# Kernel optimization log

Measured on AMD Instinct MI355X. Metric: run time of the kernel, lower is better.

The kernel has to match this reference:

```python
import jax, jax.numpy as jnp
import numpy as np

SEQ, B, I, H, O = 512, 256, 256, 512, 256


def setup_inputs() -> dict:
    key = jax.random.key(0)
    ks = jax.random.split(key, 7)
    s_ih = 1.0 / np.sqrt(H)
    return {
        "x_seq": jax.random.normal(ks[0], (SEQ, B, I), dtype=jnp.float32),
        # PyTorch LSTMCell params: gate order i, f, g, o
        "W_ih": jax.random.uniform(ks[1], (4 * H, I), jnp.float32, -s_ih, s_ih),
        "W_hh": jax.random.uniform(ks[2], (4 * H, H), jnp.float32, -s_ih, s_ih),
        "b_ih": jax.random.uniform(ks[3], (4 * H,), jnp.float32, -s_ih, s_ih),
        "b_hh": jax.random.uniform(ks[4], (4 * H,), jnp.float32, -s_ih, s_ih),
        "W_fc": jax.random.uniform(ks[5], (O, H), jnp.float32, -s_ih, s_ih),
        "b_fc": jax.random.uniform(ks[6], (O,), jnp.float32, -s_ih, s_ih),
    }


def reference(x_seq, W_ih, W_hh, b_ih, b_hh, W_fc, b_fc):
    hidden = W_hh.shape[1]
    # Precompute input projections for all timesteps at once: [S, B, 4H]
    x_proj = jnp.einsum("sbi,gi->sbg", x_seq, W_ih) + b_ih + b_hh

    def step(carry, xp_t):
        h, c = carry
        gates = xp_t + h @ W_hh.T  # [B, 4H]
        i_g, f_g, g_g, o_g = jnp.split(gates, 4, axis=-1)
        i_g = jax.nn.sigmoid(i_g)
        f_g = jax.nn.sigmoid(f_g)
        g_g = jnp.tanh(g_g)
        o_g = jax.nn.sigmoid(o_g)
        c = f_g * c + i_g * g_g
        h = o_g * jnp.tanh(c)
        return (h, c), h

    h0 = jnp.zeros((x_seq.shape[1], hidden), x_seq.dtype)
    c0 = jnp.zeros_like(h0)
    (h_f, c_f), hs = jax.lax.scan(step, (h0, c0), x_proj)
    # Linear head applied to every timestep's hidden state: [S, B, O]
    outputs = jnp.einsum("sbh,oh->sbo", hs, W_fc) + b_fc
    return outputs, (h_f, c_f)
```

## Files before the change

kernel.cpp:

```cpp
#include <hip/hip_runtime.h>
#include <math.h>

#define SEQ   512
#define BATCH 256
#define IDIM  256
#define HDIM  512
#define ODIM  256
#define NGROUP 16
#define GBLK   16

#define OUT_ELEMS ((size_t)SEQ * BATCH * ODIM)
#define HF_OFF OUT_ELEMS
#define CF_OFF (OUT_ELEMS + (size_t)BATCH * HDIM)

#define HPLANE     65536u
#define HBUFSTRIDE 131072u
#define SPIN_TIMEOUT 200000000ull

#define H_SCALE 4096.0f
#define H_INV   2.44140625e-4f
#define HMIN    6.104e-5f
#define ZW      390

typedef __attribute__((ext_vector_type(8))) _Float16 half8;
typedef __attribute__((ext_vector_type(4))) float f32x4;
typedef __attribute__((ext_vector_type(4))) unsigned int uint4v;

__device__ __forceinline__ unsigned short hbits(_Float16 h) {
  return __builtin_bit_cast(unsigned short, h);
}

__device__ __forceinline__ f32x4 mfma_h(half8 a, half8 b, f32x4 c) {
  return __builtin_amdgcn_mfma_f32_16x16x32_f16(a, b, c, 0, 0, 0);
}

__device__ __forceinline__ unsigned int ld_sys_u32(const unsigned int* p) {
  unsigned int v;
  asm volatile("global_load_dword %0, %1, off sc0 sc1\n\t"
               "s_waitcnt vmcnt(0)"
               : "=v"(v) : "v"((unsigned long long)p) : "memory");
  return v;
}

__device__ __forceinline__ void st_sys_u32(unsigned int* p, unsigned int d) {
  asm volatile("global_store_dword %0, %1, off sc0 sc1"
               : : "v"((unsigned long long)p), "v"(d) : "memory");
}

__device__ __forceinline__ void ld_2x64_sys(const unsigned int* p0, const unsigned int* p1,
                                            uint4v a[4], uint4v b[4]) {
  asm volatile(
      "global_load_dwordx4 %0, %8, off sc0 sc1\n\t"
      "global_load_dwordx4 %1, %8, off offset:16 sc0 sc1\n\t"
      "global_load_dwordx4 %2, %8, off offset:32 sc0 sc1\n\t"
      "global_load_dwordx4 %3, %8, off offset:48 sc0 sc1\n\t"
      "global_load_dwordx4 %4, %9, off sc0 sc1\n\t"
      "global_load_dwordx4 %5, %9, off offset:16 sc0 sc1\n\t"
      "global_load_dwordx4 %6, %9, off offset:32 sc0 sc1\n\t"
      "global_load_dwordx4 %7, %9, off offset:48 sc0 sc1\n\t"
      "s_waitcnt vmcnt(0)"
      : "=&v"(a[0]), "=&v"(a[1]), "=&v"(a[2]), "=&v"(a[3]),
        "=&v"(b[0]), "=&v"(b[1]), "=&v"(b[2]), "=&v"(b[3])
      : "v"((unsigned long long)p0), "v"((unsigned long long)p1)
      : "memory");
}

__device__ __forceinline__ void split_f(float f, _Float16 &hi, _Float16 &lo) {
  _Float16 a = (_Float16)0.f;
  if (fabsf(f) >= HMIN) a = (_Float16)f;
  float f1 = (float)a;
  hi = a;
  lo = (_Float16)((f - f1) * H_SCALE);
}

__device__ __forceinline__ float sigm(float x)   { return 1.f / (1.f + expf(-x)); }
__device__ __forceinline__ float tanh_f(float x) { return 1.f - 2.f / (expf(2.f * x) + 1.f); }

__device__ __forceinline__ void wait_tag(const unsigned int* tp, unsigned int tgt) {
  unsigned long long t0 = __builtin_amdgcn_s_memrealtime();
  while (ld_sys_u32(tp) < tgt) {
    if (__builtin_amdgcn_s_memrealtime() - t0 > SPIN_TIMEOUT) break;
  }
}

__global__ void __launch_bounds__(256, 1)
lstm_mfma(const float* __restrict__ xs,
          const float* __restrict__ Wih,
          const float* __restrict__ Whh,
          const float* __restrict__ bih,
          const float* __restrict__ bhh,
          const float* __restrict__ Wfc,
          const float* __restrict__ bfc,
          float* __restrict__ out,
          unsigned int* __restrict__ tags,
          unsigned int* __restrict__ hb)
{
  const int tid = threadIdx.x;
  const int w   = tid >> 6;
  const int l   = tid & 63;
  const int lr  = l & 15;
  const int lk  = l >> 4;

  const int bi  = blockIdx.x & (NGROUP - 1);
  const int gj  = blockIdx.x / NGROUP;
  const int r0  = bi * 16;
  const int hc0 = gj * 32;
  const int oc0 = gj * 16;

  half8 wz1[24][2], wz2[24][2];
#pragma unroll
  for (int kk = 0; kk < 24; ++kk)
#pragma unroll
    for (int nt = 0; nt < 2; ++nt) {
      int g = w * HDIM + hc0 + nt * 16 + lr;
      const float* src = (kk < 16)
          ? (Whh + (size_t)g * HDIM + kk * 32 + lk * 8)
          : (Wih + (size_t)g * IDIM + (kk - 16) * 32 + lk * 8);
      const f32x4 va = *(const f32x4*)src;
      const f32x4 vb = *(const f32x4*)(src + 4);
#pragma unroll
      for (int j = 0; j < 4; ++j) { _Float16 h, lo; split_f(va[j], h, lo); wz1[kk][nt][j] = h; wz2[kk][nt][j] = lo; }
#pragma unroll
      for (int j = 0; j < 4; ++j) { _Float16 h, lo; split_f(vb[j], h, lo); wz1[kk][nt][4 + j] = h; wz2[kk][nt][4 + j] = lo; }
    }
  half8 wfc1[4];
#pragma unroll
  for (int q = 0; q < 4; ++q) {
    const float* src = Wfc + (size_t)(oc0 + lr) * HDIM + (w * 4 + q) * 32 + lk * 8;
#pragma unroll
    for (int j = 0; j < 8; ++j) { _Float16 h, lo; split_f(src[j], h, lo); wfc1[q][j] = h; }
  }
  float gb[2];
#pragma unroll
  for (int nt = 0; nt < 2; ++nt) {
    int g = w * HDIM + hc0 + nt * 16 + lr;
    gb[nt] = bih[g] + bhh[g];
  }

  const int rrow = tid >> 4;
  const int rcp  = tid & 15;
  const float fcb = bfc[oc0 + rcp];

  __shared__ unsigned int z1[16][ZW];
  __shared__ unsigned int z2[16][ZW];
  __shared__ float lds_g[4][16][32];
  __shared__ float lds_fc[4][16][16];
  __shared__ float lds_c[16][32];

  lds_c[rrow][2 * rcp]     = 0.f;
  lds_c[rrow][2 * rcp + 1] = 0.f;

  const int srow = tid & 15;
  const int schk = tid >> 4;
  unsigned int* mytag = tags + (bi * 16 + schk) * 4;

#pragma unroll 1
  for (int t = 0; t < SEQ; ++t) {
    {
      const float* xt = xs + (size_t)t * BATCH * IDIM + (size_t)(r0 + srow) * IDIM + schk * 16;
#pragma unroll
      for (int i = 0; i < 8; ++i) {
        _Float16 h0, l0, h1, l1;
        split_f(xt[2 * i],     h0, l0);
        split_f(xt[2 * i + 1], h1, l1);
        int c = 256 + schk * 8 + i;
        z1[srow][c] = (unsigned int)hbits(h0) | ((unsigned int)hbits(h1) << 16);
        z2[srow][c] = (unsigned int)hbits(l0) | ((unsigned int)hbits(l1) << 16);
      }
    }

    if (t > 0) {
      wait_tag(mytag, (unsigned int)t);
      const unsigned int* p1 = hb + ((unsigned)((t - 1) & 1)) * HBUFSTRIDE
                             + (unsigned)(r0 + srow) * 256u + (unsigned)(schk * 16);
      uint4v a[4], b[4];
      ld_2x64_sys(p1, p1 + HPLANE, a, b);
#pragma unroll
      for (int j = 0; j < 4; ++j)
#pragma unroll
        for (int e = 0; e < 4; ++e) {
          z1[srow][schk * 16 + 4 * j + e] = a[j][e];
          z2[srow][schk * 16 + 4 * j + e] = b[j][e];
        }
    } else {
#pragma unroll
      for (int i = 0; i < 16; ++i) {
        z1[srow][schk * 16 + i] = 0u;
        z2[srow][schk * 16 + i] = 0u;
      }
    }
    __syncthreads();

    f32x4 ga0 = {gb[0], gb[0], gb[0], gb[0]};
    f32x4 ga1 = {gb[1], gb[1], gb[1], gb[1]};
    f32x4 gl0 = {0.f, 0.f, 0.f, 0.f};
    f32x4 gl1 = {0.f, 0.f, 0.f, 0.f};
    const unsigned short* zr1 = (const unsigned short*)&z1[lr][0];
    const unsigned short* zr2 = (const unsigned short*)&z2[lr][0];
#pragma unroll
    for (int kk = 0; kk < 24; ++kk) {
      half8 a1 = *(const half8*)(zr1 + kk * 32 + lk * 8);
      half8 a2 = *(const half8*)(zr2 + kk * 32 + lk * 8);
      ga0 = mfma_h(a1, wz1[kk][0], ga0);
      gl0 = mfma_h(a2, wz1[kk][0], gl0);
      gl0 = mfma_h(a1, wz2[kk][0], gl0);
      ga1 = mfma_h(a1, wz1[kk][1], ga1);
      gl1 = mfma_h(a2, wz1[kk][1], gl1);
      gl1 = mfma_h(a1, wz2[kk][1], gl1);
    }

    f32x4 f1a = {0.f, 0.f, 0.f, 0.f};
    f32x4 f2a = {0.f, 0.f, 0.f, 0.f};
    if (t > 0) {
#pragma unroll
      for (int q = 0; q < 4; ++q) {
        int kk = w * 4 + q;
        half8 a1 = *(const half8*)(zr1 + kk * 32 + lk * 8);
        half8 a2 = *(const half8*)(zr2 + kk * 32 + lk * 8);
        f1a = mfma_h(a1, wfc1[q], f1a);
        f2a = mfma_h(a2, wfc1[q], f2a);
      }
    }

#pragma unroll
    for (int j = 0; j < 4; ++j) {
      lds_g[w][lk * 4 + j][lr]      = ga0[j] + gl0[j] * H_INV;
      lds_g[w][lk * 4 + j][16 + lr] = ga1[j] + gl1[j] * H_INV;
      lds_fc[w][lk * 4 + j][lr]     = f1a[j] + f2a[j] * H_INV;
    }
    __syncthreads();

    float hn[2], cn[2];
#pragma unroll
    for (int q = 0; q < 2; ++q) {
      int c = 2 * rcp + q;
      float ig = sigm(lds_g[0][rrow][c]);
      float fg = sigm(lds_g[1][rrow][c]);
      float gg = tanh_f(lds_g[2][rrow][c]);
      float og = sigm(lds_g[3][rrow][c]);
      float cc = fg * lds_c[rrow][c] + ig * gg;
      lds_c[rrow][c] = cc;
      cn[q] = cc;
      hn[q] = og * tanh_f(cc);
    }

    {
      _Float16 h0h, h0l, h1h, h1l;
      split_f(hn[0], h0h, h0l);
      split_f(hn[1], h1h, h1l);
      unsigned int hiw = (unsigned int)hbits(h0h) | ((unsigned int)hbits(h1h) << 16);
      unsigned int low = (unsigned int)hbits(h0l) | ((unsigned int)hbits(h1l) << 16);
      unsigned int wi = ((unsigned)(t & 1)) * HBUFSTRIDE
                      + (unsigned)(r0 + rrow) * 256u + (unsigned)(oc0 + rcp);
      st_sys_u32(hb + wi,          hiw);
      st_sys_u32(hb + HPLANE + wi, low);
    }
    asm volatile("s_waitcnt vmcnt(0)" ::: "memory");
    __syncthreads();
    if (tid < 16) st_sys_u32(tags + (bi * 16 + tid) * 4, (unsigned int)(t + 1));

    if (t > 0) {
      float o = lds_fc[0][rrow][rcp] + lds_fc[1][rrow][rcp]
              + lds_fc[2][rrow][rcp] + lds_fc[3][rrow][rcp] + fcb;
      out[((size_t)(t - 1) * BATCH + (r0 + rrow)) * ODIM + oc0 + rcp] = o;
    }
    if (t == SEQ - 1) {
#pragma unroll
      for (int q = 0; q < 2; ++q) {
        size_t hi_ = (size_t)(r0 + rrow) * HDIM + hc0 + 2 * rcp + q;
        out[HF_OFF + hi_] = hn[q];
        out[CF_OFF + hi_] = cn[q];
      }
    }
  }

  {
    wait_tag(mytag, (unsigned int)SEQ);
    const unsigned int* p1 = hb + ((unsigned)((SEQ - 1) & 1)) * HBUFSTRIDE
                           + (unsigned)(r0 + srow) * 256u + (unsigned)(schk * 16);
    uint4v a[4], b[4];
    ld_2x64_sys(p1, p1 + HPLANE, a, b);
#pragma unroll
    for (int j = 0; j < 4; ++j)
#pragma unroll
      for (int e = 0; e < 4; ++e) {
        z1[srow][schk * 16 + 4 * j + e] = a[j][e];
        z2[srow][schk * 16 + 4 * j + e] = b[j][e];
      }
    __syncthreads();
    f32x4 f1a = {0.f, 0.f, 0.f, 0.f};
    f32x4 f2a = {0.f, 0.f, 0.f, 0.f};
    const unsigned short* zr1 = (const unsigned short*)&z1[lr][0];
    const unsigned short* zr2 = (const unsigned short*)&z2[lr][0];
#pragma unroll
    for (int q = 0; q < 4; ++q) {
      int kk = w * 4 + q;
      half8 a1 = *(const half8*)(zr1 + kk * 32 + lk * 8);
      half8 a2 = *(const half8*)(zr2 + kk * 32 + lk * 8);
      f1a = mfma_h(a1, wfc1[q], f1a);
      f2a = mfma_h(a2, wfc1[q], f2a);
    }
#pragma unroll
    for (int j = 0; j < 4; ++j)
      lds_fc[w][lk * 4 + j][lr] = f1a[j] + f2a[j] * H_INV;
    __syncthreads();
    float o = lds_fc[0][rrow][rcp] + lds_fc[1][rrow][rcp]
            + lds_fc[2][rrow][rcp] + lds_fc[3][rrow][rcp] + fcb;
    out[((size_t)(SEQ - 1) * BATCH + (r0 + rrow)) * ODIM + oc0 + rcp] = o;
  }
}

extern "C" void kernel_launch(void* const* d_in, const int* in_sizes, int n_in,
                              void* d_out, int out_size, void* d_ws, size_t ws_size,
                              hipStream_t stream)
{
  const float* xs  = (const float*)d_in[0];
  const float* wih = (const float*)d_in[1];
  const float* whh = (const float*)d_in[2];
  const float* bi_ = (const float*)d_in[3];
  const float* bh_ = (const float*)d_in[4];
  const float* wfc = (const float*)d_in[5];
  const float* bf_ = (const float*)d_in[6];
  float* out = (float*)d_out;

  unsigned int* tags = (unsigned int*)d_ws;
  unsigned int* hb   = (unsigned int*)((char*)d_ws + 4096);

  hipMemsetAsync(d_ws, 0, 4096, stream);

  lstm_mfma<<<dim3(NGROUP * GBLK), dim3(256), 0, stream>>>(
      xs, wih, whh, bi_, bh_, wfc, bf_, out, tags, hb);
}
```

Baseline: 4.956 ms.

## Replace tag-based grid sync with sentinel-polled triple-buffered hidden state

Drops the per-step tag flags and barrier-then-flag protocol. Consumers now poll the hidden-state slab itself until no word equals a sentinel value, and three rotating buffers are used so that the slot two steps ahead can be reset to the sentinel. The input-projection MFMAs for the x part are issued before waiting on h, overlapping that compute with the cross-block dependency. The x loads are also vectorised. This relies on a real fp16 pair never matching the sentinel bit pattern and on stores being visible in the right order across blocks.

```diff
diff --git a/kernel.cpp b/kernel.cpp
--- a/kernel.cpp
+++ b/kernel.cpp
@@ -13,8 +13,9 @@
 #define HF_OFF OUT_ELEMS
 #define CF_OFF (OUT_ELEMS + (size_t)BATCH * HDIM)
 
-#define HPLANE     65536u
-#define HBUFSTRIDE 131072u
+#define HPLANE 65536u
+#define BUFW   131072u
+#define SENT   0x7F7F7F7Fu
 #define SPIN_TIMEOUT 200000000ull
 
 #define H_SCALE 4096.0f
@@ -32,14 +33,6 @@
 
 __device__ __forceinline__ f32x4 mfma_h(half8 a, half8 b, f32x4 c) {
   return __builtin_amdgcn_mfma_f32_16x16x32_f16(a, b, c, 0, 0, 0);
-}
-
-__device__ __forceinline__ unsigned int ld_sys_u32(const unsigned int* p) {
-  unsigned int v;
-  asm volatile("global_load_dword %0, %1, off sc0 sc1\n\t"
-               "s_waitcnt vmcnt(0)"
-               : "=v"(v) : "v"((unsigned long long)p) : "memory");
-  return v;
 }
 
 __device__ __forceinline__ void st_sys_u32(unsigned int* p, unsigned int d) {
@@ -65,6 +58,24 @@
       : "memory");
 }
 
+__device__ __forceinline__ void poll_slab(const unsigned int* p0, const unsigned int* p1,
+                                          uint4v a[4], uint4v b[4]) {
+  unsigned long long t0 = __builtin_amdgcn_s_memrealtime();
+  for (;;) {
+    ld_2x64_sys(p0, p1, a, b);
+    unsigned int bad = 0;
+#pragma unroll
+    for (int j = 0; j < 4; ++j)
+#pragma unroll
+      for (int e = 0; e < 4; ++e) {
+        bad |= (a[j][e] == SENT);
+        bad |= (b[j][e] == SENT);
+      }
+    if (!bad) return;
+    if (__builtin_amdgcn_s_memrealtime() - t0 > SPIN_TIMEOUT) return;
+  }
+}
+
 __device__ __forceinline__ void split_f(float f, _Float16 &hi, _Float16 &lo) {
   _Float16 a = (_Float16)0.f;
   if (fabsf(f) >= HMIN) a = (_Float16)f;
@@ -75,13 +86,6 @@
 
 __device__ __forceinline__ float sigm(float x)   { return 1.f / (1.f + expf(-x)); }
 __device__ __forceinline__ float tanh_f(float x) { return 1.f - 2.f / (expf(2.f * x) + 1.f); }
-
-__device__ __forceinline__ void wait_tag(const unsigned int* tp, unsigned int tgt) {
-  unsigned long long t0 = __builtin_amdgcn_s_memrealtime();
-  while (ld_sys_u32(tp) < tgt) {
-    if (__builtin_amdgcn_s_memrealtime() - t0 > SPIN_TIMEOUT) break;
-  }
-}
 
 __global__ void __launch_bounds__(256, 1)
 lstm_mfma(const float* __restrict__ xs,
@@ -92,7 +96,6 @@
           const float* __restrict__ Wfc,
           const float* __restrict__ bfc,
           float* __restrict__ out,
-          unsigned int* __restrict__ tags,
           unsigned int* __restrict__ hb)
 {
   const int tid = threadIdx.x;
@@ -140,6 +143,7 @@
   const int rrow = tid >> 4;
   const int rcp  = tid & 15;
   const float fcb = bfc[oc0 + rcp];
+  const unsigned int wi_row = (unsigned)(r0 + rrow) * 256u + (unsigned)(oc0 + rcp);
 
   __shared__ unsigned int z1[16][ZW];
   __shared__ unsigned int z2[16][ZW];
@@ -152,41 +156,26 @@
 
   const int srow = tid & 15;
   const int schk = tid >> 4;
-  unsigned int* mytag = tags + (bi * 16 + schk) * 4;
+
+  unsigned int* pR = hb + 2u * BUFW;
+  unsigned int* pW = hb;
+  unsigned int* pS = hb + BUFW;
 
 #pragma unroll 1
   for (int t = 0; t < SEQ; ++t) {
     {
       const float* xt = xs + (size_t)t * BATCH * IDIM + (size_t)(r0 + srow) * IDIM + schk * 16;
 #pragma unroll
-      for (int i = 0; i < 8; ++i) {
-        _Float16 h0, l0, h1, l1;
-        split_f(xt[2 * i],     h0, l0);
-        split_f(xt[2 * i + 1], h1, l1);
-        int c = 256 + schk * 8 + i;
-        z1[srow][c] = (unsigned int)hbits(h0) | ((unsigned int)hbits(h1) << 16);
-        z2[srow][c] = (unsigned int)hbits(l0) | ((unsigned int)hbits(l1) << 16);
-      }
-    }
-
-    if (t > 0) {
-      wait_tag(mytag, (unsigned int)t);
-      const unsigned int* p1 = hb + ((unsigned)((t - 1) & 1)) * HBUFSTRIDE
-                             + (unsigned)(r0 + srow) * 256u + (unsigned)(schk * 16);
-      uint4v a[4], b[4];
-      ld_2x64_sys(p1, p1 + HPLANE, a, b);
-#pragma unroll
-      for (int j = 0; j < 4; ++j)
-#pragma unroll
-        for (int e = 0; e < 4; ++e) {
-          z1[srow][schk * 16 + 4 * j + e] = a[j][e];
-          z2[srow][schk * 16 + 4 * j + e] = b[j][e];
-        }
-    } else {
-#pragma unroll
-      for (int i = 0; i < 16; ++i) {
-        z1[srow][schk * 16 + i] = 0u;
-        z2[srow][schk * 16 + i] = 0u;
+      for (int v4 = 0; v4 < 4; ++v4) {
+        f32x4 xv = *(const f32x4*)(xt + 4 * v4);
+        _Float16 h0, l0, h1, l1, h2, l2, h3, l3;
+        split_f(xv[0], h0, l0); split_f(xv[1], h1, l1);
+        split_f(xv[2], h2, l2); split_f(xv[3], h3, l3);
+        int c = 256 + schk * 8 + 2 * v4;
+        z1[srow][c]     = (unsigned int)hbits(h0) | ((unsigned int)hbits(h1) << 16);
+        z2[srow][c]     = (unsigned int)hbits(l0) | ((unsigned int)hbits(l1) << 16);
+        z1[srow][c + 1] = (unsigned int)hbits(h2) | ((unsigned int)hbits(h3) << 16);
+        z2[srow][c + 1] = (unsigned int)hbits(l2) | ((unsigned int)hbits(l3) << 16);
       }
     }
     __syncthreads();
@@ -198,7 +187,7 @@
     const unsigned short* zr1 = (const unsigned short*)&z1[lr][0];
     const unsigned short* zr2 = (const unsigned short*)&z2[lr][0];
 #pragma unroll
-    for (int kk = 0; kk < 24; ++kk) {
+    for (int kk = 16; kk < 24; ++kk) {
       half8 a1 = *(const half8*)(zr1 + kk * 32 + lk * 8);
       half8 a2 = *(const half8*)(zr2 + kk * 32 + lk * 8);
       ga0 = mfma_h(a1, wz1[kk][0], ga0);
@@ -207,6 +196,36 @@
       ga1 = mfma_h(a1, wz1[kk][1], ga1);
       gl1 = mfma_h(a2, wz1[kk][1], gl1);
       gl1 = mfma_h(a1, wz2[kk][1], gl1);
+    }
+
+    if (t > 0) {
+      const unsigned int* p1 = pR + (unsigned)(r0 + srow) * 256u + (unsigned)(schk * 16);
+      uint4v a[4], b[4];
+      poll_slab(p1, p1 + HPLANE, a, b);
+#pragma unroll
+      for (int j = 0; j < 4; ++j)
+#pragma unroll
+        for (int e = 0; e < 4; ++e) {
+          z1[srow][schk * 16 + 4 * j + e] = a[j][e];
+          z2[srow][schk * 16 + 4 * j + e] = b[j][e];
+        }
+    }
+    st_sys_u32(pS + wi_row,          SENT);
+    st_sys_u32(pS + HPLANE + wi_row, SENT);
+    __syncthreads();
+
+    if (t > 0) {
+#pragma unroll
+      for (int kk = 0; kk < 16; ++kk) {
+        half8 a1 = *(const half8*)(zr1 + kk * 32 + lk * 8);
+        half8 a2 = *(const half8*)(zr2 + kk * 32 + lk * 8);
+        ga0 = mfma_h(a1, wz1[kk][0], ga0);
+        gl0 = mfma_h(a2, wz1[kk][0], gl0);
+        gl0 = mfma_h(a1, wz2[kk][0], gl0);
+        ga1 = mfma_h(a1, wz1[kk][1], ga1);
+        gl1 = mfma_h(a2, wz1[kk][1], gl1);
+        gl1 = mfma_h(a1, wz2[kk][1], gl1);
+      }
     }
 
     f32x4 f1a = {0.f, 0.f, 0.f, 0.f};
@@ -244,20 +263,16 @@
       hn[q] = og * tanh_f(cc);
     }
 
+    asm volatile("s_waitcnt vmcnt(0)" ::: "memory");
     {
       _Float16 h0h, h0l, h1h, h1l;
       split_f(hn[0], h0h, h0l);
       split_f(hn[1], h1h, h1l);
       unsigned int hiw = (unsigned int)hbits(h0h) | ((unsigned int)hbits(h1h) << 16);
       unsigned int low = (unsigned int)hbits(h0l) | ((unsigned int)hbits(h1l) << 16);
-      unsigned int wi = ((unsigned)(t & 1)) * HBUFSTRIDE
-                      + (unsigned)(r0 + rrow) * 256u + (unsigned)(oc0 + rcp);
-      st_sys_u32(hb + wi,          hiw);
-      st_sys_u32(hb + HPLANE + wi, low);
-    }
-    asm volatile("s_waitcnt vmcnt(0)" ::: "memory");
-    __syncthreads();
-    if (tid < 16) st_sys_u32(tags + (bi * 16 + tid) * 4, (unsigned int)(t + 1));
+      st_sys_u32(pW + wi_row,          hiw);
+      st_sys_u32(pW + HPLANE + wi_row, low);
+    }
 
     if (t > 0) {
       float o = lds_fc[0][rrow][rcp] + lds_fc[1][rrow][rcp]
@@ -272,14 +287,14 @@
         out[CF_OFF + hi_] = cn[q];
       }
     }
+
+    unsigned int* tmp = pR; pR = pW; pW = pS; pS = tmp;
   }
 
   {
-    wait_tag(mytag, (unsigned int)SEQ);
-    const unsigned int* p1 = hb + ((unsigned)((SEQ - 1) & 1)) * HBUFSTRIDE
-                           + (unsigned)(r0 + srow) * 256u + (unsigned)(schk * 16);
+    const unsigned int* p1 = pR + (unsigned)(r0 + srow) * 256u + (unsigned)(schk * 16);
     uint4v a[4], b[4];
-    ld_2x64_sys(p1, p1 + HPLANE, a, b);
+    poll_slab(p1, p1 + HPLANE, a, b);
 #pragma unroll
     for (int j = 0; j < 4; ++j)
 #pragma unroll
@@ -323,11 +338,10 @@
   const float* bf_ = (const float*)d_in[6];
   float* out = (float*)d_out;
 
-  unsigned int* tags = (unsigned int*)d_ws;
-  unsigned int* hb   = (unsigned int*)((char*)d_ws + 4096);
-
-  hipMemsetAsync(d_ws, 0, 4096, stream);
+  unsigned int* hb = (unsigned int*)d_ws;
+
+  hipMemsetAsync(hb, 0x7F, (size_t)3 * BUFW * 4, stream);
 
   lstm_mfma<<<dim3(NGROUP * GBLK), dim3(256), 0, stream>>>(
-      xs, wih, whh, bi_, bh_, wfc, bf_, out, tags, hb);
-}
+      xs, wih, whh, bi_, bh_, wfc, bf_, out, hb);
+}
```

After: 4.891 ms. About the same (-1.3%).
